# Performance work log

Measured on AMD Instinct MI355X. Metric: run time of the kernel, lower is better.

Reference implementation:

```python
import jax, jax.numpy as jnp
import numpy as np

N = 1024
X_DIM = 128
Y_DIM = 128
HIDDEN = 256


def setup_inputs() -> dict:
    key = jax.random.key(0)
    ks = jax.random.split(key, 6)
    x_samples = jax.random.normal(ks[0], (N, X_DIM), dtype=jnp.float32)
    y_samples = jax.random.normal(ks[1], (N, Y_DIM), dtype=jnp.float32)
    in_dim = X_DIM + Y_DIM
    # Linear params (kaiming-uniform-ish small init)
    W1 = jax.random.normal(ks[2], (in_dim, HIDDEN), dtype=jnp.float32) / np.sqrt(in_dim)
    b1 = jnp.zeros((HIDDEN,), dtype=jnp.float32)
    W2 = jax.random.normal(ks[3], (HIDDEN, 1), dtype=jnp.float32) / np.sqrt(HIDDEN)
    b2 = jnp.zeros((1,), dtype=jnp.float32)
    return {"x_samples": x_samples, "y_samples": y_samples,
            "W1": W1, "b1": b1, "W2": W2, "b2": b2}


def reference(x_samples, y_samples, W1, b1, W2, b2):
    n = y_samples.shape[0]
    W1x, W1y = W1[:X_DIM], W1[X_DIM:]
    xp = x_samples @ W1x          # [N, H]  (x_tile[i, j] = x[j])
    yp = y_samples @ W1y          # [N, H]  (y_tile[i, j] = y[i])
    # T0: F(cat([x_i, y_i])) on the diagonal pairs -> [N, 1]
    T0 = jax.nn.relu(xp + yp + b1) @ W2 + b2
    # T1: F over all pairs (i, j) -> [N, N, 1]
    h = jax.nn.relu(yp[:, None, :] + xp[None, :, :] + b1)   # [N, N, H]
    T1 = h @ W2 + b2                                        # [N, N, 1]
    lse = jax.scipy.special.logsumexp(T1, axis=1)           # [N, 1] over dim=1
    lower_bound = T0.mean() - (lse.mean() - jnp.log(jnp.float32(n)))
    return lower_bound
```

## Files before the change

### kernel.cpp

```cpp
#include <hip/hip_runtime.h>

#define N_SAMP 1024
#define XD     128
#define HID    256


__global__ __launch_bounds__(256) void gemm_xy(
    const float* __restrict__ x, const float* __restrict__ y,
    const float* __restrict__ W1, const float* __restrict__ b1,
    float* __restrict__ xpbT, float* __restrict__ ypT,
    float* __restrict__ S, float* __restrict__ T0sum)
{
    const int k  = threadIdx.x;
    const int r0 = blockIdx.x * 4;

    if (threadIdx.x < 4) S[blockIdx.x * 4 + threadIdx.x] = 0.f;
    if (blockIdx.x == 0 && threadIdx.x == 4) T0sum[0] = 0.f;
    if (blockIdx.x == 0 && threadIdx.x == 5) ((unsigned*)T0sum)[1] = 0u;

    float ax0 = 0.f, ax1 = 0.f, ax2 = 0.f, ax3 = 0.f;
    float ay0 = 0.f, ay1 = 0.f, ay2 = 0.f, ay3 = 0.f;

    #pragma unroll 4
    for (int d = 0; d < XD; ++d) {
        const float wx = W1[d * HID + k];
        const float wy = W1[(XD + d) * HID + k];
        ax0 = fmaf(x[(r0 + 0) * XD + d], wx, ax0);
        ax1 = fmaf(x[(r0 + 1) * XD + d], wx, ax1);
        ax2 = fmaf(x[(r0 + 2) * XD + d], wx, ax2);
        ax3 = fmaf(x[(r0 + 3) * XD + d], wx, ax3);
        ay0 = fmaf(y[(r0 + 0) * XD + d], wy, ay0);
        ay1 = fmaf(y[(r0 + 1) * XD + d], wy, ay1);
        ay2 = fmaf(y[(r0 + 2) * XD + d], wy, ay2);
        ay3 = fmaf(y[(r0 + 3) * XD + d], wy, ay3);
    }

    const float bk = b1[k];
    float4 xs4 = make_float4(ax0 + bk, ax1 + bk, ax2 + bk, ax3 + bk);
    float4 ys4 = make_float4(ay0, ay1, ay2, ay3);
    *(float4*)&xpbT[k * N_SAMP + r0] = xs4;
    *(float4*)&ypT [k * N_SAMP + r0] = ys4;
}

__global__ __launch_bounds__(256) void pair_fused(
    const float* __restrict__ ypT, const float* __restrict__ xpbT,
    const float* __restrict__ W2,
    float* __restrict__ S, float* __restrict__ T0s,
    const float* __restrict__ b2, float* __restrict__ out)
{
    __shared__ float xs[64][64];
    __shared__ float ys[64][64];
    __shared__ float wlds[HID];

    const int tid = threadIdx.x;
    const int tj  = tid & 15;
    const int ti  = tid >> 4;
    const int jb  = blockIdx.x * 64;
    const int ib  = blockIdx.y * 64;
    const int j0  = jb + tj * 4;
    const int i0  = ib + ti * 4;
    const int tj4 = tj * 4, ti4 = ti * 4;

    if (tid < 64) *(float4*)&wlds[tid * 4] = *(const float4*)&W2[tid * 4];

    float acc[4][4];
    #pragma unroll
    for (int a = 0; a < 4; ++a)
        #pragma unroll
        for (int b = 0; b < 4; ++b) acc[a][b] = 0.f;

    for (int pass = 0; pass < 4; ++pass) {
        const int kof = pass << 6;
        if (pass) __syncthreads();

        #pragma unroll
        for (int s = 0; s < 4; ++s) {
            const int f  = s * 256 + tid;
            const int kk = f >> 4;
            const int q  = (f & 15) * 4;
            *(float4*)&xs[kk][q] = *(const float4*)&xpbT[(kof + kk) * N_SAMP + jb + q];
            *(float4*)&ys[kk][q] = *(const float4*)&ypT [(kof + kk) * N_SAMP + ib + q];
        }
        __syncthreads();

        #pragma unroll 2
        for (int c = 0; c < 8; ++c) {
            const int kb = c * 8;
            const float4 wa = *(const float4*)&wlds[kof + kb];
            const float4 wb = *(const float4*)&wlds[kof + kb + 4];
            const float wv[8] = {wa.x, wa.y, wa.z, wa.w,
                                 wb.x, wb.y, wb.z, wb.w};
            #pragma unroll
            for (int u = 0; u < 8; ++u) {
                const int kk = kb + u;
                const float4 xv = *(const float4*)&xs[kk][tj4];
                const float4 yv = *(const float4*)&ys[kk][ti4];
                const float xa[4] = {xv.x, xv.y, xv.z, xv.w};
                const float ya[4] = {yv.x, yv.y, yv.z, yv.w};
                #pragma unroll
                for (int a = 0; a < 4; ++a)
                    #pragma unroll
                    for (int b = 0; b < 4; ++b)
                        acc[a][b] = fmaf(fmaxf(ya[a] + xa[b], 0.f),
                                         wv[u], acc[a][b]);
            }
        }
    }

    #pragma unroll
    for (int a = 0; a < 4; ++a) {
        float e = __expf(acc[a][0]) + __expf(acc[a][1])
                + __expf(acc[a][2]) + __expf(acc[a][3]);
        #pragma unroll
        for (int off = 8; off; off >>= 1) e += __shfl_xor(e, off, 16);
        if (tj == 0) atomicAdd(&S[i0 + a], e);
    }

    if (blockIdx.x == blockIdx.y) {
        float dv = 0.f;
        if (ti == tj)
            dv = acc[0][0] + acc[1][1] + acc[2][2] + acc[3][3];
        #pragma unroll
        for (int off = 32; off; off >>= 1) dv += __shfl_xor(dv, off, 64);
        if ((tid & 63) == 0) atomicAdd(&T0s[0], dv);
    }

    int* lastflag = (int*)&ys[0][0];
    __threadfence();
    __syncthreads();
    if (tid == 0)
        *lastflag = (atomicAdd((unsigned*)&T0s[1], 1u) == 255u);
    __syncthreads();
    if (!*lastflag) return;

    float* red = &xs[0][0];
    float ls = 0.f;
    for (int i = tid; i < N_SAMP; i += 256)
        ls += logf(atomicAdd(&S[i], 0.f));
    #pragma unroll
    for (int off = 32; off; off >>= 1) ls += __shfl_xor(ls, off, 64);
    if ((tid & 63) == 0) red[tid >> 6] = ls;
    __syncthreads();

    if (tid == 0) {
        const float t0       = atomicAdd(&T0s[0], 0.f);
        const float lse_sum  = red[0] + red[1] + red[2] + red[3];
        const float t0_mean  = t0 / (float)N_SAMP + b2[0];
        const float lse_mean = lse_sum / (float)N_SAMP + b2[0]
                             - logf((float)N_SAMP);
        out[0] = t0_mean - lse_mean;
    }
}

extern "C" void kernel_launch(void* const* d_in, const int* in_sizes, int n_in,
                              void* d_out, int out_size, void* d_ws, size_t ws_size,
                              hipStream_t stream)
{
    const float* x  = (const float*)d_in[0];
    const float* y  = (const float*)d_in[1];
    const float* W1 = (const float*)d_in[2];
    const float* b1 = (const float*)d_in[3];
    const float* W2 = (const float*)d_in[4];
    const float* b2 = (const float*)d_in[5];

    float* ws   = (float*)d_ws;
    float* S    = ws;
    float* T0s  = ws + 1024;
    float* xpbT = ws + 2048;
    float* ypT  = ws + 2048 + HID * N_SAMP;

    gemm_xy   <<<dim3(N_SAMP / 4), dim3(256), 0, stream>>>(x, y, W1, b1,
                                                           xpbT, ypT, S, T0s);
    pair_fused<<<dim3(16, 16),     dim3(256), 0, stream>>>(ypT, xpbT, W2,
                                                           S, T0s, b2,
                                                           (float*)d_out);
}
```

Measured before the change: 120.9 us.

## Shrink pair tile to 16x64 per block for more blocks and less LDS

The pair kernel now gives each thread a 1x4 output strip instead of a 4x4 tile. Blocks cover 16 rows by 64 columns, so the grid has 1024 blocks instead of 256. The y tile in shared memory shrinks, and launch bounds ask for 4 blocks per CU. The aim is better occupancy and a fuller spread of work over the MI355X CUs. The cost is less register reuse: each x load from LDS now feeds only 4 FMAs instead of 16, which can make LDS bandwidth the limit and adds more S atomics.

```diff
diff --git a/kernel.cpp b/kernel.cpp
--- a/kernel.cpp
+++ b/kernel.cpp
@@ -42,33 +42,30 @@
     *(float4*)&ypT [k * N_SAMP + r0] = ys4;
 }
 
-__global__ __launch_bounds__(256) void pair_fused(
+__global__ __launch_bounds__(256, 4) void pair_fused(
     const float* __restrict__ ypT, const float* __restrict__ xpbT,
     const float* __restrict__ W2,
     float* __restrict__ S, float* __restrict__ T0s,
     const float* __restrict__ b2, float* __restrict__ out)
 {
     __shared__ float xs[64][64];
-    __shared__ float ys[64][64];
+    __shared__ float ys[64][16];
     __shared__ float wlds[HID];
 
     const int tid = threadIdx.x;
     const int tj  = tid & 15;
     const int ti  = tid >> 4;
     const int jb  = blockIdx.x * 64;
-    const int ib  = blockIdx.y * 64;
+    const int ib  = blockIdx.y * 16;
     const int j0  = jb + tj * 4;
-    const int i0  = ib + ti * 4;
-    const int tj4 = tj * 4, ti4 = ti * 4;
+    const int i0  = ib + ti;
+    const int tj4 = tj * 4;
 
     if (tid < 64) *(float4*)&wlds[tid * 4] = *(const float4*)&W2[tid * 4];
 
-    float acc[4][4];
-    #pragma unroll
-    for (int a = 0; a < 4; ++a)
-        #pragma unroll
-        for (int b = 0; b < 4; ++b) acc[a][b] = 0.f;
+    float a0 = 0.f, a1 = 0.f, a2 = 0.f, a3 = 0.f;
 
+    #pragma unroll 1
     for (int pass = 0; pass < 4; ++pass) {
         const int kof = pass << 6;
         if (pass) __syncthreads();
@@ -79,47 +76,45 @@
             const int kk = f >> 4;
             const int q  = (f & 15) * 4;
             *(float4*)&xs[kk][q] = *(const float4*)&xpbT[(kof + kk) * N_SAMP + jb + q];
-            *(float4*)&ys[kk][q] = *(const float4*)&ypT [(kof + kk) * N_SAMP + ib + q];
+        }
+        {
+            const int kk = tid >> 2;
+            const int q  = (tid & 3) * 4;
+            *(float4*)&ys[kk][q] = *(const float4*)&ypT[(kof + kk) * N_SAMP + ib + q];
         }
         __syncthreads();
 
-        #pragma unroll 2
-        for (int c = 0; c < 8; ++c) {
-            const int kb = c * 8;
-            const float4 wa = *(const float4*)&wlds[kof + kb];
-            const float4 wb = *(const float4*)&wlds[kof + kb + 4];
-            const float wv[8] = {wa.x, wa.y, wa.z, wa.w,
-                                 wb.x, wb.y, wb.z, wb.w};
+        #pragma unroll
+        for (int c = 0; c < 16; ++c) {
+            const float4 wv = *(const float4*)&wlds[kof + c * 4];
+            const float wu[4] = {wv.x, wv.y, wv.z, wv.w};
             #pragma unroll
-            for (int u = 0; u < 8; ++u) {
-                const int kk = kb + u;
+            for (int u = 0; u < 4; ++u) {
+                const int kk = c * 4 + u;
                 const float4 xv = *(const float4*)&xs[kk][tj4];
-                const float4 yv = *(const float4*)&ys[kk][ti4];
-                const float xa[4] = {xv.x, xv.y, xv.z, xv.w};
-                const float ya[4] = {yv.x, yv.y, yv.z, yv.w};
-                #pragma unroll
-                for (int a = 0; a < 4; ++a)
-                    #pragma unroll
-                    for (int b = 0; b < 4; ++b)
-                        acc[a][b] = fmaf(fmaxf(ya[a] + xa[b], 0.f),
-                                         wv[u], acc[a][b]);
+                const float  yv = ys[kk][ti];
+                a0 = fmaf(fmaxf(yv + xv.x, 0.f), wu[u], a0);
+                a1 = fmaf(fmaxf(yv + xv.y, 0.f), wu[u], a1);
+                a2 = fmaf(fmaxf(yv + xv.z, 0.f), wu[u], a2);
+                a3 = fmaf(fmaxf(yv + xv.w, 0.f), wu[u], a3);
             }
         }
     }
 
-    #pragma unroll
-    for (int a = 0; a < 4; ++a) {
-        float e = __expf(acc[a][0]) + __expf(acc[a][1])
-                + __expf(acc[a][2]) + __expf(acc[a][3]);
+    {
+        float e = __expf(a0) + __expf(a1) + __expf(a2) + __expf(a3);
         #pragma unroll
         for (int off = 8; off; off >>= 1) e += __shfl_xor(e, off, 16);
-        if (tj == 0) atomicAdd(&S[i0 + a], e);
+        if (tj == 0) atomicAdd(&S[i0], e);
     }
 
-    if (blockIdx.x == blockIdx.y) {
+    if ((int)blockIdx.x == (int)(blockIdx.y >> 2)) {
+        const int d = i0 - j0;
         float dv = 0.f;
-        if (ti == tj)
-            dv = acc[0][0] + acc[1][1] + acc[2][2] + acc[3][3];
+        if      (d == 0) dv = a0;
+        else if (d == 1) dv = a1;
+        else if (d == 2) dv = a2;
+        else if (d == 3) dv = a3;
         #pragma unroll
         for (int off = 32; off; off >>= 1) dv += __shfl_xor(dv, off, 64);
         if ((tid & 63) == 0) atomicAdd(&T0s[0], dv);
@@ -129,7 +124,7 @@
     __threadfence();
     __syncthreads();
     if (tid == 0)
-        *lastflag = (atomicAdd((unsigned*)&T0s[1], 1u) == 255u);
+        *lastflag = (atomicAdd((unsigned*)&T0s[1], 1u) == 1023u);
     __syncthreads();
     if (!*lastflag) return;
 
@@ -171,7 +166,7 @@
 
     gemm_xy   <<<dim3(N_SAMP / 4), dim3(256), 0, stream>>>(x, y, W1, b1,
                                                            xpbT, ypT, S, T0s);
-    pair_fused<<<dim3(16, 16),     dim3(256), 0, stream>>>(ypT, xpbT, W2,
+    pair_fused<<<dim3(16, 64),     dim3(256), 0, stream>>>(ypT, xpbT, W2,
                                                            S, T0s, b2,
                                                            (float*)d_out);
 }
```

Result: slower. 159.1 us (+31.6%).
